# Kernel optimization log

Hardware: AMD Instinct MI355X
Metric: run time of the kernel (lower is better)

The kernel has to match this reference:

```python
import jax, jax.numpy as jnp
import numpy as np

N_NODES = 81
N_EDGES = 1620
IN_DIM = 10
HIDDEN = 8192
ACTIONS = 729


def setup_inputs() -> dict:
    key = jax.random.key(0)
    ks = jax.random.split(key, 8)
    x = jax.random.normal(ks[0], (N_NODES, IN_DIM), dtype=jnp.float32)
    edge_index = jax.random.randint(ks[1], (2, N_EDGES), 0, N_NODES, dtype=jnp.int64)
    W_gcn = jax.random.normal(ks[2], (IN_DIM, HIDDEN), dtype=jnp.float32) / np.sqrt(IN_DIM)
    b_gcn = jnp.zeros((HIDDEN,), dtype=jnp.float32)
    ln_g = jnp.ones((HIDDEN,), dtype=jnp.float32)
    ln_b = jnp.zeros((HIDDEN,), dtype=jnp.float32)
    W1 = jax.random.normal(ks[3], (HIDDEN, HIDDEN), dtype=jnp.float32) / np.sqrt(HIDDEN)
    b1 = jnp.zeros((HIDDEN,), dtype=jnp.float32)
    W2 = jax.random.normal(ks[4], (HIDDEN, ACTIONS), dtype=jnp.float32) / np.sqrt(HIDDEN)
    b2 = jnp.zeros((ACTIONS,), dtype=jnp.float32)
    return {"x": x, "edge_index": edge_index, "W_gcn": W_gcn, "b_gcn": b_gcn,
            "ln_g": ln_g, "ln_b": ln_b, "W1": W1, "b1": b1, "W2": W2, "b2": b2}


def _gcn_conv(x, edge_index, W, b):
    # GCNConv with added self-loops and symmetric D^-1/2 (A+I) D^-1/2 normalization
    n = x.shape[0]
    loops = jnp.arange(n, dtype=edge_index.dtype)
    src = jnp.concatenate([edge_index[0], loops])  # [E+N]
    dst = jnp.concatenate([edge_index[1], loops])
    h = x @ W  # [N, H] — transform before propagate, as in PyG
    deg = jnp.zeros((n,), dtype=h.dtype).at[dst].add(1.0)
    dinv = jnp.where(deg > 0, jax.lax.rsqrt(deg), 0.0)
    norm = dinv[src] * dinv[dst]  # [E+N]
    msg = h[src] * norm[:, None]
    out = jnp.zeros_like(h).at[dst].add(msg)
    return out + b


def _layer_norm(h, g, b, eps=1e-5):
    mu = jnp.mean(h, axis=-1, keepdims=True)
    var = jnp.mean(jnp.square(h - mu), axis=-1, keepdims=True)
    return (h - mu) * jax.lax.rsqrt(var + eps) * g + b


def reference(x, edge_index, W_gcn, b_gcn, ln_g, ln_b, W1, b1, W2, b2):
    h = jax.nn.relu(_gcn_conv(x, edge_index, W_gcn, b_gcn))  # [81, H]
    h = _layer_norm(h, ln_g, ln_b)
    # global_add_pool with batch = zeros(81): sum all nodes into one graph row
    g = jnp.sum(h, axis=0, keepdims=True)  # [1, H]
    g = jax.nn.relu(g @ W1 + b1)
    logits = g @ W2 + b2  # [1, ACTIONS]
    return jax.nn.log_softmax(logits, axis=1)
```

## Files before the change

kernel.cpp:

```cpp
#include <hip/hip_runtime.h>
#include <math.h>

#define N_NODES 81
#define N_EDGES 1620
#define IN_DIM 10
#define HIDDEN 8192
#define ACTIONS 729
#define NT_CH 92

__global__ __launch_bounds__(256) void stats_kernel(const float* __restrict__ x,
                                                    const int* __restrict__ ei,
                                                    const float* __restrict__ Wg,
                                                    const float* __restrict__ bg,
                                                    float* __restrict__ yr_all,
                                                    float* __restrict__ stats,
                                                    float* __restrict__ logits,
                                                    unsigned* __restrict__ counter) {
    const int n = blockIdx.x;
    const int t = threadIdx.x;
    __shared__ float deg[N_NODES];
    __shared__ float yr[IN_DIM];
    __shared__ float red[8];

    if (t < N_NODES) deg[t] = 1.0f;
    if (t < IN_DIM) yr[t] = 0.0f;
    __syncthreads();
    for (int e = t; e < N_EDGES; e += 256) atomicAdd(&deg[ei[N_EDGES + e]], 1.0f);
    __syncthreads();
    if (t < N_NODES) deg[t] = rsqrtf(deg[t]);
    __syncthreads();
    const float dn = deg[n];
    for (int e = t; e < N_EDGES; e += 256) {
        if (ei[N_EDGES + e] == n) {
            int s = ei[e];
            float nrm = deg[s] * dn;
            #pragma unroll
            for (int c = 0; c < IN_DIM; ++c) atomicAdd(&yr[c], nrm * x[s * IN_DIM + c]);
        }
    }
    if (t == 0) {
        float nrm = dn * dn;
        #pragma unroll
        for (int c = 0; c < IN_DIM; ++c) atomicAdd(&yr[c], nrm * x[n * IN_DIM + c]);
    }
    __syncthreads();
    if (t < IN_DIM) yr_all[n * IN_DIM + t] = yr[t];
    if (n == 0) {
        for (int a = t; a < ACTIONS; a += 256) logits[a] = 0.f;
        if (t == 0) *counter = 0u;
    }

    const float4* Wg4 = (const float4*)Wg;
    const float4* bg4 = (const float4*)bg;
    float s = 0.f, s2 = 0.f;
    #pragma unroll
    for (int k = 0; k < 8; ++k) {
        int j4 = t + k * 256;
        float4 h = bg4[j4];
        #pragma unroll
        for (int c = 0; c < IN_DIM; ++c) {
            float4 w = Wg4[c * (HIDDEN / 4) + j4];
            float yc = yr[c];
            h.x = fmaf(yc, w.x, h.x);
            h.y = fmaf(yc, w.y, h.y);
            h.z = fmaf(yc, w.z, h.z);
            h.w = fmaf(yc, w.w, h.w);
        }
        h.x = fmaxf(h.x, 0.f); h.y = fmaxf(h.y, 0.f);
        h.z = fmaxf(h.z, 0.f); h.w = fmaxf(h.w, 0.f);
        s  += h.x + h.y + h.z + h.w;
        s2 += h.x * h.x + h.y * h.y + h.z * h.z + h.w * h.w;
    }
    #pragma unroll
    for (int off = 32; off > 0; off >>= 1) { s += __shfl_xor(s, off); s2 += __shfl_xor(s2, off); }
    int wave = t >> 6, lane = t & 63;
    if (lane == 0) { red[wave] = s; red[4 + wave] = s2; }
    __syncthreads();
    if (t == 0) {
        float S  = red[0] + red[1] + red[2] + red[3];
        float S2 = red[4] + red[5] + red[6] + red[7];
        float mu = S * (1.f / HIDDEN);
        float var = S2 * (1.f / HIDDEN) - mu * mu;
        stats[2 * n]     = mu;
        stats[2 * n + 1] = rsqrtf(var + 1e-5f);
    }
}

__global__ __launch_bounds__(256) void gemv1_kernel(const float* __restrict__ Wg,
                                                    const float* __restrict__ bg,
                                                    const float* __restrict__ lng,
                                                    const float* __restrict__ lnb,
                                                    const float* __restrict__ yr_all,
                                                    const float* __restrict__ stats,
                                                    const float* __restrict__ W1,
                                                    float* __restrict__ partial) {
    const int ch = blockIdx.x;
    const int ct = blockIdx.y;
    const int row0 = ch * 64;
    const int t = threadIdx.x;

    __shared__ float syr[N_NODES * IN_DIM];
    __shared__ float sstat[2 * N_NODES];
    __shared__ float sw[IN_DIM][64];
    __shared__ float gred[4][64];
    __shared__ float gl[64];

    for (int i = t; i < N_NODES * IN_DIM; i += 256) syr[i] = yr_all[i];
    for (int i = t; i < 2 * N_NODES; i += 256) sstat[i] = stats[i];
    if (t < 64) {
        #pragma unroll
        for (int c = 0; c < IN_DIM; ++c) sw[c][t] = Wg[c * HIDDEN + row0 + t];
    }
    __syncthreads();

    {
        const int r = t & 63, grp = t >> 6;
        const float bgv = bg[row0 + r];
        float acc = 0.f;
        for (int n = grp; n < N_NODES; n += 4) {
            float h = bgv;
            #pragma unroll
            for (int c = 0; c < IN_DIM; ++c) h = fmaf(syr[n * IN_DIM + c], sw[c][r], h);
            h = fmaxf(h, 0.f);
            acc += (h - sstat[2 * n]) * sstat[2 * n + 1];
        }
        gred[grp][r] = acc;
    }
    __syncthreads();
    if (t < 64)
        gl[t] = (gred[0][t] + gred[1][t] + gred[2][t] + gred[3][t]) * lng[row0 + t]
                + (float)N_NODES * lnb[row0 + t];
    __syncthreads();

    float4 acc = make_float4(0.f, 0.f, 0.f, 0.f);
    const float* pbase = W1 + (size_t)row0 * HIDDEN + ct * 1024 + t * 4;
    if (ch >= NT_CH) {
        #pragma unroll 8
        for (int i = 0; i < 64; ++i) {
            const float* q = pbase + (size_t)i * HIDDEN;
            float4 w;
            w.x = __builtin_nontemporal_load(q);
            w.y = __builtin_nontemporal_load(q + 1);
            w.z = __builtin_nontemporal_load(q + 2);
            w.w = __builtin_nontemporal_load(q + 3);
            float gi = gl[i];
            acc.x = fmaf(gi, w.x, acc.x);
            acc.y = fmaf(gi, w.y, acc.y);
            acc.z = fmaf(gi, w.z, acc.z);
            acc.w = fmaf(gi, w.w, acc.w);
        }
    } else {
        const float4* p = (const float4*)(pbase);
        #pragma unroll 8
        for (int i = 0; i < 64; ++i) {
            float4 w = p[(size_t)i * (HIDDEN / 4)];
            float gi = gl[i];
            acc.x = fmaf(gi, w.x, acc.x);
            acc.y = fmaf(gi, w.y, acc.y);
            acc.z = fmaf(gi, w.z, acc.z);
            acc.w = fmaf(gi, w.w, acc.w);
        }
    }
    ((float4*)(partial + (size_t)ch * HIDDEN + ct * 1024))[t] = acc;
}

__global__ __launch_bounds__(256) void gemv2_lsm_kernel(const float* __restrict__ partial,
                                                        const float* __restrict__ b1,
                                                        const float* __restrict__ W2,
                                                        const float* __restrict__ b2,
                                                        float* __restrict__ logits,
                                                        unsigned* __restrict__ counter,
                                                        float* __restrict__ out) {
    const int ch = blockIdx.x;
    const int row0 = ch * 32;
    const int t = threadIdx.x;
    __shared__ float sred[8][32];
    __shared__ float gl[32];
    __shared__ int isLast;

    {
        const int r = t & 31, grp = t >> 5;
        float a = 0.f;
        #pragma unroll 4
        for (int c = grp; c < 128; c += 8) a += partial[(size_t)c * HIDDEN + row0 + r];
        sred[grp][r] = a;
    }
    __syncthreads();
    if (t < 32) {
        float S = b1[row0 + t];
        #pragma unroll
        for (int gq = 0; gq < 8; ++gq) S += sred[gq][t];
        gl[t] = fmaxf(S, 0.f);
    }
    __syncthreads();

    float s0 = 0.f, s1 = 0.f, s2v = 0.f;
    const bool has2 = (t + 512) < ACTIONS;
    #pragma unroll 4
    for (int i = 0; i < 32; ++i) {
        float gi = gl[i];
        const float* r = W2 + (size_t)(row0 + i) * ACTIONS;
        s0 = fmaf(gi, r[t], s0);
        s1 = fmaf(gi, r[t + 256], s1);
        if (has2) s2v = fmaf(gi, r[t + 512], s2v);
    }
    atomicAdd(&logits[t], s0);
    atomicAdd(&logits[t + 256], s1);
    if (has2) atomicAdd(&logits[t + 512], s2v);

    asm volatile("s_waitcnt vmcnt(0)" ::: "memory");
    __syncthreads();
    if (t == 0) isLast = (atomicAdd(counter, 1u) == 255u) ? 1 : 0;
    __syncthreads();

    if (isLast) {
        float l0 = __hip_atomic_load(&logits[t], __ATOMIC_RELAXED,
                                     __HIP_MEMORY_SCOPE_AGENT) + b2[t];
        float l1 = __hip_atomic_load(&logits[t + 256], __ATOMIC_RELAXED,
                                     __HIP_MEMORY_SCOPE_AGENT) + b2[t + 256];
        float l2 = has2 ? (__hip_atomic_load(&logits[t + 512], __ATOMIC_RELAXED,
                                             __HIP_MEMORY_SCOPE_AGENT) + b2[t + 512])
                        : -INFINITY;
        float m = fmaxf(fmaxf(l0, l1), l2);
        #pragma unroll
        for (int off = 32; off > 0; off >>= 1) m = fmaxf(m, __shfl_xor(m, off));
        if ((t & 63) == 0) sred[0][t >> 6] = m;
        __syncthreads();
        float M = fmaxf(fmaxf(sred[0][0], sred[0][1]), fmaxf(sred[0][2], sred[0][3]));
        __syncthreads();
        float e = __expf(l0 - M) + __expf(l1 - M) + (has2 ? __expf(l2 - M) : 0.f);
        #pragma unroll
        for (int off = 32; off > 0; off >>= 1) e += __shfl_xor(e, off);
        if ((t & 63) == 0) sred[0][t >> 6] = e;
        __syncthreads();
        float Se = sred[0][0] + sred[0][1] + sred[0][2] + sred[0][3];
        float L = logf(Se);
        out[t] = l0 - M - L;
        out[t + 256] = l1 - M - L;
        if (has2) out[t + 512] = l2 - M - L;
    }
}

extern "C" void kernel_launch(void* const* d_in, const int* in_sizes, int n_in,
                              void* d_out, int out_size, void* d_ws, size_t ws_size,
                              hipStream_t stream) {
    const float* x    = (const float*)d_in[0];
    const int*   ei   = (const int*)  d_in[1];
    const float* Wg   = (const float*)d_in[2];
    const float* bg   = (const float*)d_in[3];
    const float* lng  = (const float*)d_in[4];
    const float* lnb  = (const float*)d_in[5];
    const float* W1   = (const float*)d_in[6];
    const float* b1   = (const float*)d_in[7];
    const float* W2   = (const float*)d_in[8];
    const float* b2   = (const float*)d_in[9];
    float* out = (float*)d_out;

    float* ws = (float*)d_ws;
    float* logits    = ws;
    unsigned* counter = (unsigned*)(ws + 1024);
    float* stats   = ws + 1088;
    float* yr_all  = ws + 1280;
    float* partial = ws + 4096;

    stats_kernel<<<N_NODES, 256, 0, stream>>>(x, ei, Wg, bg, yr_all, stats, logits, counter);
    gemv1_kernel<<<dim3(128, 8), 256, 0, stream>>>(Wg, bg, lng, lnb, yr_all, stats, W1, partial);
    gemv2_lsm_kernel<<<256, 256, 0, stream>>>(partial, b1, W2, b2, logits, counter, out);
}
```

Baseline: 89.83 us.

## Split stats kernel across hidden tiles and reduce gemv1 partials with atomics

Launches the stats kernel over 8 hidden-dimension tiles per node, raising the block count from 81 to 648. Each block writes partial sum and sum-of-squares, and gemv1 combines them into mean and rstd. gemv1 now atomically adds its per-chunk results into one 8192-wide vector, which the stats kernel zeroes first. This removes the 128x8192 partial buffer and the read-and-reduce step at the start of gemv2. The cost is recomputing degree and aggregation 8 times per node, plus atomic contention from 128 chunks per output element.

```diff
diff --git a/kernel.cpp b/kernel.cpp
--- a/kernel.cpp
+++ b/kernel.cpp
@@ -13,10 +13,13 @@
                                                     const float* __restrict__ Wg,
                                                     const float* __restrict__ bg,
                                                     float* __restrict__ yr_all,
-                                                    float* __restrict__ stats,
+                                                    float* __restrict__ stats_part,
                                                     float* __restrict__ logits,
-                                                    unsigned* __restrict__ counter) {
-    const int n = blockIdx.x;
+                                                    unsigned* __restrict__ ctr,
+                                                    float* __restrict__ g2a) {
+    const int bid = blockIdx.x;
+    const int n = bid >> 3;
+    const int jt = bid & 7;
     const int t = threadIdx.x;
     __shared__ float deg[N_NODES];
     __shared__ float yr[IN_DIM];
@@ -44,45 +47,42 @@
         for (int c = 0; c < IN_DIM; ++c) atomicAdd(&yr[c], nrm * x[n * IN_DIM + c]);
     }
     __syncthreads();
-    if (t < IN_DIM) yr_all[n * IN_DIM + t] = yr[t];
-    if (n == 0) {
+    if (jt == 0 && t < IN_DIM) yr_all[n * IN_DIM + t] = yr[t];
+    if (bid == 0) {
         for (int a = t; a < ACTIONS; a += 256) logits[a] = 0.f;
-        if (t == 0) *counter = 0u;
+        if (t == 0) *ctr = 0u;
+    }
+    if (bid >= 1 && bid <= 8) {
+        const int base = (bid - 1) * 1024;
+        #pragma unroll
+        for (int k = 0; k < 4; ++k) g2a[base + t + k * 256] = 0.f;
     }
 
     const float4* Wg4 = (const float4*)Wg;
     const float4* bg4 = (const float4*)bg;
-    float s = 0.f, s2 = 0.f;
+    const int j4 = jt * 256 + t;
+    float4 h = bg4[j4];
     #pragma unroll
-    for (int k = 0; k < 8; ++k) {
-        int j4 = t + k * 256;
-        float4 h = bg4[j4];
-        #pragma unroll
-        for (int c = 0; c < IN_DIM; ++c) {
-            float4 w = Wg4[c * (HIDDEN / 4) + j4];
-            float yc = yr[c];
-            h.x = fmaf(yc, w.x, h.x);
-            h.y = fmaf(yc, w.y, h.y);
-            h.z = fmaf(yc, w.z, h.z);
-            h.w = fmaf(yc, w.w, h.w);
-        }
-        h.x = fmaxf(h.x, 0.f); h.y = fmaxf(h.y, 0.f);
-        h.z = fmaxf(h.z, 0.f); h.w = fmaxf(h.w, 0.f);
-        s  += h.x + h.y + h.z + h.w;
-        s2 += h.x * h.x + h.y * h.y + h.z * h.z + h.w * h.w;
-    }
+    for (int c = 0; c < IN_DIM; ++c) {
+        float4 w = Wg4[c * (HIDDEN / 4) + j4];
+        float yc = yr[c];
+        h.x = fmaf(yc, w.x, h.x);
+        h.y = fmaf(yc, w.y, h.y);
+        h.z = fmaf(yc, w.z, h.z);
+        h.w = fmaf(yc, w.w, h.w);
+    }
+    h.x = fmaxf(h.x, 0.f); h.y = fmaxf(h.y, 0.f);
+    h.z = fmaxf(h.z, 0.f); h.w = fmaxf(h.w, 0.f);
+    float s  = h.x + h.y + h.z + h.w;
+    float s2 = h.x * h.x + h.y * h.y + h.z * h.z + h.w * h.w;
     #pragma unroll
     for (int off = 32; off > 0; off >>= 1) { s += __shfl_xor(s, off); s2 += __shfl_xor(s2, off); }
     int wave = t >> 6, lane = t & 63;
     if (lane == 0) { red[wave] = s; red[4 + wave] = s2; }
     __syncthreads();
     if (t == 0) {
-        float S  = red[0] + red[1] + red[2] + red[3];
-        float S2 = red[4] + red[5] + red[6] + red[7];
-        float mu = S * (1.f / HIDDEN);
-        float var = S2 * (1.f / HIDDEN) - mu * mu;
-        stats[2 * n]     = mu;
-        stats[2 * n + 1] = rsqrtf(var + 1e-5f);
+        stats_part[n * 16 + jt * 2]     = red[0] + red[1] + red[2] + red[3];
+        stats_part[n * 16 + jt * 2 + 1] = red[4] + red[5] + red[6] + red[7];
     }
 }
 
@@ -91,25 +91,36 @@
                                                     const float* __restrict__ lng,
                                                     const float* __restrict__ lnb,
                                                     const float* __restrict__ yr_all,
-                                                    const float* __restrict__ stats,
+                                                    const float* __restrict__ stats_part,
                                                     const float* __restrict__ W1,
-                                                    float* __restrict__ partial) {
+                                                    float* __restrict__ g2a) {
     const int ch = blockIdx.x;
     const int ct = blockIdx.y;
     const int row0 = ch * 64;
     const int t = threadIdx.x;
 
     __shared__ float syr[N_NODES * IN_DIM];
+    __shared__ float spart[N_NODES * 16];
     __shared__ float sstat[2 * N_NODES];
     __shared__ float sw[IN_DIM][64];
     __shared__ float gred[4][64];
     __shared__ float gl[64];
 
     for (int i = t; i < N_NODES * IN_DIM; i += 256) syr[i] = yr_all[i];
-    for (int i = t; i < 2 * N_NODES; i += 256) sstat[i] = stats[i];
+    for (int i = t; i < N_NODES * 16; i += 256) spart[i] = stats_part[i];
     if (t < 64) {
         #pragma unroll
         for (int c = 0; c < IN_DIM; ++c) sw[c][t] = Wg[c * HIDDEN + row0 + t];
+    }
+    __syncthreads();
+    if (t < N_NODES) {
+        float S = 0.f, S2 = 0.f;
+        #pragma unroll
+        for (int j = 0; j < 8; ++j) { S += spart[t * 16 + 2 * j]; S2 += spart[t * 16 + 2 * j + 1]; }
+        float mu = S * (1.f / HIDDEN);
+        float var = S2 * (1.f / HIDDEN) - mu * mu;
+        sstat[2 * t]     = mu;
+        sstat[2 * t + 1] = rsqrtf(var + 1e-5f);
     }
     __syncthreads();
 
@@ -150,7 +161,7 @@
             acc.w = fmaf(gi, w.w, acc.w);
         }
     } else {
-        const float4* p = (const float4*)(pbase);
+        const float4* p = (const float4*)pbase;
         #pragma unroll 8
         for (int i = 0; i < 64; ++i) {
             float4 w = p[(size_t)i * (HIDDEN / 4)];
@@ -161,10 +172,14 @@
             acc.w = fmaf(gi, w.w, acc.w);
         }
     }
-    ((float4*)(partial + (size_t)ch * HIDDEN + ct * 1024))[t] = acc;
-}
-
-__global__ __launch_bounds__(256) void gemv2_lsm_kernel(const float* __restrict__ partial,
+    float* q0 = g2a + ct * 1024 + t * 4;
+    atomicAdd(q0 + 0, acc.x);
+    atomicAdd(q0 + 1, acc.y);
+    atomicAdd(q0 + 2, acc.z);
+    atomicAdd(q0 + 3, acc.w);
+}
+
+__global__ __launch_bounds__(256) void gemv2_lsm_kernel(const float* __restrict__ g2a,
                                                         const float* __restrict__ b1,
                                                         const float* __restrict__ W2,
                                                         const float* __restrict__ b2,
@@ -174,24 +189,11 @@
     const int ch = blockIdx.x;
     const int row0 = ch * 32;
     const int t = threadIdx.x;
-    __shared__ float sred[8][32];
     __shared__ float gl[32];
+    __shared__ float red[8];
     __shared__ int isLast;
 
-    {
-        const int r = t & 31, grp = t >> 5;
-        float a = 0.f;
-        #pragma unroll 4
-        for (int c = grp; c < 128; c += 8) a += partial[(size_t)c * HIDDEN + row0 + r];
-        sred[grp][r] = a;
-    }
-    __syncthreads();
-    if (t < 32) {
-        float S = b1[row0 + t];
-        #pragma unroll
-        for (int gq = 0; gq < 8; ++gq) S += sred[gq][t];
-        gl[t] = fmaxf(S, 0.f);
-    }
+    if (t < 32) gl[t] = fmaxf(g2a[row0 + t] + b1[row0 + t], 0.f);
     __syncthreads();
 
     float s0 = 0.f, s1 = 0.f, s2v = 0.f;
@@ -224,16 +226,16 @@
         float m = fmaxf(fmaxf(l0, l1), l2);
         #pragma unroll
         for (int off = 32; off > 0; off >>= 1) m = fmaxf(m, __shfl_xor(m, off));
-        if ((t & 63) == 0) sred[0][t >> 6] = m;
+        if ((t & 63) == 0) red[t >> 6] = m;
         __syncthreads();
-        float M = fmaxf(fmaxf(sred[0][0], sred[0][1]), fmaxf(sred[0][2], sred[0][3]));
+        float M = fmaxf(fmaxf(red[0], red[1]), fmaxf(red[2], red[3]));
         __syncthreads();
         float e = __expf(l0 - M) + __expf(l1 - M) + (has2 ? __expf(l2 - M) : 0.f);
         #pragma unroll
         for (int off = 32; off > 0; off >>= 1) e += __shfl_xor(e, off);
-        if ((t & 63) == 0) sred[0][t >> 6] = e;
+        if ((t & 63) == 0) red[t >> 6] = e;
         __syncthreads();
-        float Se = sred[0][0] + sred[0][1] + sred[0][2] + sred[0][3];
+        float Se = red[0] + red[1] + red[2] + red[3];
         float L = logf(Se);
         out[t] = l0 - M - L;
         out[t + 256] = l1 - M - L;
@@ -257,13 +259,15 @@
     float* out = (float*)d_out;
 
     float* ws = (float*)d_ws;
-    float* logits    = ws;
+    float* logits     = ws;
     unsigned* counter = (unsigned*)(ws + 1024);
-    float* stats   = ws + 1088;
-    float* yr_all  = ws + 1280;
-    float* partial = ws + 4096;
-
-    stats_kernel<<<N_NODES, 256, 0, stream>>>(x, ei, Wg, bg, yr_all, stats, logits, counter);
-    gemv1_kernel<<<dim3(128, 8), 256, 0, stream>>>(Wg, bg, lng, lnb, yr_all, stats, W1, partial);
-    gemv2_lsm_kernel<<<256, 256, 0, stream>>>(partial, b1, W2, b2, logits, counter, out);
-}
+    float* stats_part = ws + 1088;
+    float* yr_all     = ws + 2384;
+    float* g2a        = ws + 4096;
+
+    stats_kernel<<<N_NODES * 8, 256, 0, stream>>>(x, ei, Wg, bg, yr_all, stats_part,
+                                                  logits, counter, g2a);
+    gemv1_kernel<<<dim3(128, 8), 256, 0, stream>>>(Wg, bg, lng, lnb, yr_all,
+                                                   stats_part, W1, g2a);
+    gemv2_lsm_kernel<<<256, 256, 0, stream>>>(g2a, b1, W2, b2, logits, counter, out);
+}
```

New measurement: 99.11 us. +10.3%, slower.

## Materialize normalized node features in first kernel and prefetch W1 rows early

Applied to the files above, without the earlier changes.

The first kernel now writes the full layer-normalized, gamma-scaled hidden matrix [81, 8192] to workspace, replacing the small per-node stats and aggregated inputs. The GEMV1 kernel then only sums columns of this matrix instead of recomputing the GCN transform per block. It also issues the first 8 rows of W1 loads before the pooling reduction so they overlap with it. The trade-off is about 2.6 MB of extra global write and read traffic, which replaces redundant compute that each of the 1024 blocks previously repeated.

```diff
diff --git a/kernel.cpp b/kernel.cpp
--- a/kernel.cpp
+++ b/kernel.cpp
@@ -8,14 +8,14 @@
 #define ACTIONS 729
 #define NT_CH 92
 
-__global__ __launch_bounds__(256) void stats_kernel(const float* __restrict__ x,
-                                                    const int* __restrict__ ei,
-                                                    const float* __restrict__ Wg,
-                                                    const float* __restrict__ bg,
-                                                    float* __restrict__ yr_all,
-                                                    float* __restrict__ stats,
-                                                    float* __restrict__ logits,
-                                                    unsigned* __restrict__ counter) {
+__global__ __launch_bounds__(256) void k1_kernel(const float* __restrict__ x,
+                                                 const int* __restrict__ ei,
+                                                 const float* __restrict__ Wg,
+                                                 const float* __restrict__ bg,
+                                                 const float* __restrict__ lng,
+                                                 float* __restrict__ hn,
+                                                 float* __restrict__ logits,
+                                                 unsigned* __restrict__ counter) {
     const int n = blockIdx.x;
     const int t = threadIdx.x;
     __shared__ float deg[N_NODES];
@@ -44,7 +44,6 @@
         for (int c = 0; c < IN_DIM; ++c) atomicAdd(&yr[c], nrm * x[n * IN_DIM + c]);
     }
     __syncthreads();
-    if (t < IN_DIM) yr_all[n * IN_DIM + t] = yr[t];
     if (n == 0) {
         for (int a = t; a < ACTIONS; a += 256) logits[a] = 0.f;
         if (t == 0) *counter = 0u;
@@ -52,6 +51,8 @@
 
     const float4* Wg4 = (const float4*)Wg;
     const float4* bg4 = (const float4*)bg;
+    const float4* lng4 = (const float4*)lng;
+    float4 hv[8];
     float s = 0.f, s2 = 0.f;
     #pragma unroll
     for (int k = 0; k < 8; ++k) {
@@ -68,6 +69,7 @@
         }
         h.x = fmaxf(h.x, 0.f); h.y = fmaxf(h.y, 0.f);
         h.z = fmaxf(h.z, 0.f); h.w = fmaxf(h.w, 0.f);
+        hv[k] = h;
         s  += h.x + h.y + h.z + h.w;
         s2 += h.x * h.x + h.y * h.y + h.z * h.z + h.w * h.w;
     }
@@ -76,22 +78,28 @@
     int wave = t >> 6, lane = t & 63;
     if (lane == 0) { red[wave] = s; red[4 + wave] = s2; }
     __syncthreads();
-    if (t == 0) {
-        float S  = red[0] + red[1] + red[2] + red[3];
-        float S2 = red[4] + red[5] + red[6] + red[7];
-        float mu = S * (1.f / HIDDEN);
-        float var = S2 * (1.f / HIDDEN) - mu * mu;
-        stats[2 * n]     = mu;
-        stats[2 * n + 1] = rsqrtf(var + 1e-5f);
-    }
-}
-
-__global__ __launch_bounds__(256) void gemv1_kernel(const float* __restrict__ Wg,
-                                                    const float* __restrict__ bg,
-                                                    const float* __restrict__ lng,
-                                                    const float* __restrict__ lnb,
-                                                    const float* __restrict__ yr_all,
-                                                    const float* __restrict__ stats,
+    float S  = red[0] + red[1] + red[2] + red[3];
+    float S2 = red[4] + red[5] + red[6] + red[7];
+    float mu = S * (1.f / HIDDEN);
+    float var = S2 * (1.f / HIDDEN) - mu * mu;
+    float inv = rsqrtf(var + 1e-5f);
+    float4* hn4 = (float4*)hn + (size_t)n * (HIDDEN / 4);
+    #pragma unroll
+    for (int k = 0; k < 8; ++k) {
+        int j4 = t + k * 256;
+        float4 h = hv[k];
+        float4 g = lng4[j4];
+        float4 o;
+        o.x = (h.x - mu) * inv * g.x;
+        o.y = (h.y - mu) * inv * g.y;
+        o.z = (h.z - mu) * inv * g.z;
+        o.w = (h.w - mu) * inv * g.w;
+        hn4[j4] = o;
+    }
+}
+
+__global__ __launch_bounds__(256) void gemv1_kernel(const float* __restrict__ lnb,
+                                                    const float* __restrict__ hn,
                                                     const float* __restrict__ W1,
                                                     float* __restrict__ partial) {
     const int ch = blockIdx.x;
@@ -99,44 +107,53 @@
     const int row0 = ch * 64;
     const int t = threadIdx.x;
 
-    __shared__ float syr[N_NODES * IN_DIM];
-    __shared__ float sstat[2 * N_NODES];
-    __shared__ float sw[IN_DIM][64];
     __shared__ float gred[4][64];
     __shared__ float gl[64];
 
-    for (int i = t; i < N_NODES * IN_DIM; i += 256) syr[i] = yr_all[i];
-    for (int i = t; i < 2 * N_NODES; i += 256) sstat[i] = stats[i];
-    if (t < 64) {
-        #pragma unroll
-        for (int c = 0; c < IN_DIM; ++c) sw[c][t] = Wg[c * HIDDEN + row0 + t];
-    }
-    __syncthreads();
+    const float* pbase = W1 + (size_t)row0 * HIDDEN + ct * 1024 + t * 4;
+
+    float4 pre[8];
+    if (ch >= NT_CH) {
+        #pragma unroll
+        for (int i = 0; i < 8; ++i) {
+            const float* q = pbase + (size_t)i * HIDDEN;
+            pre[i].x = __builtin_nontemporal_load(q);
+            pre[i].y = __builtin_nontemporal_load(q + 1);
+            pre[i].z = __builtin_nontemporal_load(q + 2);
+            pre[i].w = __builtin_nontemporal_load(q + 3);
+        }
+    } else {
+        const float4* p = (const float4*)pbase;
+        #pragma unroll
+        for (int i = 0; i < 8; ++i) pre[i] = p[(size_t)i * (HIDDEN / 4)];
+    }
 
     {
         const int r = t & 63, grp = t >> 6;
-        const float bgv = bg[row0 + r];
-        float acc = 0.f;
-        for (int n = grp; n < N_NODES; n += 4) {
-            float h = bgv;
-            #pragma unroll
-            for (int c = 0; c < IN_DIM; ++c) h = fmaf(syr[n * IN_DIM + c], sw[c][r], h);
-            h = fmaxf(h, 0.f);
-            acc += (h - sstat[2 * n]) * sstat[2 * n + 1];
-        }
-        gred[grp][r] = acc;
+        float a = 0.f;
+        #pragma unroll 3
+        for (int n = grp; n < N_NODES; n += 4)
+            a += hn[(size_t)n * HIDDEN + row0 + r];
+        gred[grp][r] = a;
     }
     __syncthreads();
     if (t < 64)
-        gl[t] = (gred[0][t] + gred[1][t] + gred[2][t] + gred[3][t]) * lng[row0 + t]
+        gl[t] = gred[0][t] + gred[1][t] + gred[2][t] + gred[3][t]
                 + (float)N_NODES * lnb[row0 + t];
     __syncthreads();
 
     float4 acc = make_float4(0.f, 0.f, 0.f, 0.f);
-    const float* pbase = W1 + (size_t)row0 * HIDDEN + ct * 1024 + t * 4;
+    #pragma unroll
+    for (int i = 0; i < 8; ++i) {
+        float gi = gl[i];
+        acc.x = fmaf(gi, pre[i].x, acc.x);
+        acc.y = fmaf(gi, pre[i].y, acc.y);
+        acc.z = fmaf(gi, pre[i].z, acc.z);
+        acc.w = fmaf(gi, pre[i].w, acc.w);
+    }
     if (ch >= NT_CH) {
         #pragma unroll 8
-        for (int i = 0; i < 64; ++i) {
+        for (int i = 8; i < 64; ++i) {
             const float* q = pbase + (size_t)i * HIDDEN;
             float4 w;
             w.x = __builtin_nontemporal_load(q);
@@ -150,9 +167,9 @@
             acc.w = fmaf(gi, w.w, acc.w);
         }
     } else {
-        const float4* p = (const float4*)(pbase);
+        const float4* p = (const float4*)pbase;
         #pragma unroll 8
-        for (int i = 0; i < 64; ++i) {
+        for (int i = 8; i < 64; ++i) {
             float4 w = p[(size_t)i * (HIDDEN / 4)];
             float gi = gl[i];
             acc.x = fmaf(gi, w.x, acc.x);
@@ -257,13 +274,12 @@
     float* out = (float*)d_out;
 
     float* ws = (float*)d_ws;
-    float* logits    = ws;
+    float* logits     = ws;
     unsigned* counter = (unsigned*)(ws + 1024);
-    float* stats   = ws + 1088;
-    float* yr_all  = ws + 1280;
-    float* partial = ws + 4096;
-
-    stats_kernel<<<N_NODES, 256, 0, stream>>>(x, ei, Wg, bg, yr_all, stats, logits, counter);
-    gemv1_kernel<<<dim3(128, 8), 256, 0, stream>>>(Wg, bg, lng, lnb, yr_all, stats, W1, partial);
+    float* hn         = ws + 4096;
+    float* partial    = ws + 4096 + 663552;
+
+    k1_kernel<<<N_NODES, 256, 0, stream>>>(x, ei, Wg, bg, lng, hn, logits, counter);
+    gemv1_kernel<<<dim3(128, 8), 256, 0, stream>>>(lnb, hn, W1, partial);
     gemv2_lsm_kernel<<<256, 256, 0, stream>>>(partial, b1, W2, b2, logits, counter, out);
 }
```

Result: slower. 93.26 us (+3.8%).
